# Performance work log

Hardware: AMD Instinct MI355X
Metric: run time of the kernel (lower is better)

## Reference

```python
import jax, jax.numpy as jnp
import numpy as np

B, NL2, NRC, NIN = 32768, 4, 8, 41
NCTRL = NIN + NL2 + NIN  # 86


def _blur(n):
    # tridiagonal blur: 0.8 on diag, 0.1 on the two off-diagonals (symmetric)
    return 0.8 * jnp.eye(n, dtype=jnp.float32) \
         + 0.1 * jnp.eye(n, k=1, dtype=jnp.float32) \
         + 0.1 * jnp.eye(n, k=-1, dtype=jnp.float32)


def _leaky(x):
    return jnp.where(x >= 0, x, 0.2 * x)  # LeakyReLU(0.2)


def _passgate(w, b, rc, x):
    # w: [B,out,in,rc] clamped to [-1,1]; rc: [B,rc]; x: [B,in] -> [B,out]
    w2 = jnp.einsum('boir,br->boi', jnp.clip(w, -1.0, 1.0), rc)
    return jnp.einsum('boi,bi->bo', w2, x) + b


def setup_inputs() -> dict:
    key = jax.random.key(0)
    ks = jax.random.split(key, 4)
    s_f = np.float32(np.sqrt(2.0 / (NIN * NRC)))
    s_r = np.float32(np.sqrt(2.0 / (NL2 * NRC)))
    inp = jax.random.normal(ks[0], (B, NIN), dtype=jnp.float32)
    fpg_w = jnp.clip(jax.random.normal(ks[1], (B, NL2, NIN, NRC), dtype=jnp.float32) * s_f, -1.0, 1.0)
    rpg_w = jnp.clip(jax.random.normal(ks[2], (B, NIN, NL2, NRC), dtype=jnp.float32) * s_r, -1.0, 1.0)
    fpg_b = jnp.zeros((B, NL2), dtype=jnp.float32)
    rpg_b = jnp.zeros((B, NIN), dtype=jnp.float32)
    # pgctrl: shared nn.Linear(86, 8) (default torch init ~ U(-1/sqrt(86), 1/sqrt(86)))
    bound = np.float32(1.0 / np.sqrt(NCTRL))
    kw, kb = jax.random.split(ks[3])
    pgctrl_w = jax.random.uniform(kw, (NRC, NCTRL), dtype=jnp.float32, minval=-bound, maxval=bound)
    pgctrl_b = jax.random.uniform(kb, (NRC,), dtype=jnp.float32, minval=-bound, maxval=bound)
    return {"inp": inp, "fpg_w": fpg_w, "fpg_b": fpg_b,
            "rpg_w": rpg_w, "rpg_b": rpg_b,
            "pgctrl_w": pgctrl_w, "pgctrl_b": pgctrl_b}


def reference(inp, fpg_w, fpg_b, rpg_w, rpg_b, pgctrl_w, pgctrl_b):
    rcblur = _blur(NRC)   # [8,8]
    l2blur = _blur(NL2)   # [4,4]
    # initial state buffers are zeros; note l2old/rcold are NOT updated inside
    # the outer loop (faithful to the original), only l1i carries over.
    l2old = jnp.zeros((B, NL2), dtype=inp.dtype)
    rcold = jnp.zeros((B, NRC), dtype=inp.dtype)
    l1i = jnp.zeros((B, NIN), dtype=inp.dtype)
    l2 = l2old
    rc = rcold
    for _ in range(2):
        rcin = jnp.concatenate([inp, l2old, inp - l1i], axis=1)  # [B,86]
        rc = _leaky(rcin @ pgctrl_w.T + pgctrl_b)
        rc = jnp.clip(0.4 * rc + 0.6 * rcold, -0.2, 1.0)
        for _ in range(3):
            rc = rc @ rcblur.T
        l2 = _passgate(fpg_w, fpg_b, rc, inp) * 0.1 + 0.9 * l2old
        l2 = jnp.clip(l2, -0.2, 1.0)
        for _ in range(2):
            l2 = l2 @ l2blur.T
        l1i = jnp.clip(_passgate(rpg_w, rpg_b, rc, l2), -0.2, 1.0)
    return (l1i, l2, rc)
```

## Files before the change

kernel.cpp:

```cpp
#include <hip/hip_runtime.h>

#define B_ROWS 32768
#define NIN 41
#define NL2 4
#define NRC 8

__device__ __forceinline__ float clampf(float v, float lo, float hi) {
    return fminf(fmaxf(v, lo), hi);
}

__device__ __forceinline__ float clamp1(float v) {
    return fminf(fmaxf(v, -1.f), 1.f);
}

template <int Ctrl>
__device__ __forceinline__ int dpp_add(int x) {
    return __float_as_int(
        __int_as_float(x) +
        __int_as_float(__builtin_amdgcn_update_dpp(0, x, Ctrl, 0xf, 0xf, true)));
}

__device__ __forceinline__ float wave_sum_uniform(float v) {
    int x = __float_as_int(v);
    x = dpp_add<0x111>(x);
    x = dpp_add<0x112>(x);
    x = dpp_add<0x114>(x);
    x = dpp_add<0x118>(x);
    x = dpp_add<0x142>(x);
    x = dpp_add<0x143>(x);
    return __int_as_float(__builtin_amdgcn_readlane(x, 63));
}

__global__ void __launch_bounds__(256, 4) pgnet_kernel(
    const float* __restrict__ inp,
    const float* __restrict__ fpg_w,
    const float* __restrict__ fpg_b,
    const float* __restrict__ rpg_w,
    const float* __restrict__ rpg_b,
    const float* __restrict__ pgw,
    const float* __restrict__ pgb,
    float* __restrict__ out)
{
    const int lane = threadIdx.x & 63;
    const int row  = blockIdx.x * 4 + (threadIdx.x >> 6);
    const bool act = lane < NIN;
    const int safe = act ? lane : (NIN - 1);

    const float x_raw = inp[row * NIN + safe];

    const float* fp = fpg_w + (size_t)row * 1312 + (size_t)safe * 8;
    float4 fwv[NL2][2];
    #pragma unroll
    for (int o = 0; o < NL2; ++o) {
        fwv[o][0] = *(const float4*)(fp + o * 328);
        fwv[o][1] = *(const float4*)(fp + o * 328 + 4);
    }

    const float* rp = rpg_w + (size_t)row * 1312 + (size_t)safe * 32;
    float4 rwv[8];
    #pragma unroll
    for (int j = 0; j < 8; ++j) rwv[j] = ((const float4*)rp)[j];

    float w1r[NRC], w2r[NRC];
    #pragma unroll
    for (int r = 0; r < NRC; ++r) {
        w1r[r] = pgw[r * 86 + safe];
        w2r[r] = pgw[r * 86 + 45 + safe];
    }

    const float4 fbv  = *(const float4*)(fpg_b + (size_t)row * NL2);
    const float  rb_r = rpg_b[row * NIN + safe];

    __builtin_amdgcn_sched_barrier(0);

    const float x  = act ? x_raw : 0.0f;
    const float rb = act ? rb_r  : 0.0f;

    float fw[NL2][NRC];
    #pragma unroll
    for (int o = 0; o < NL2; ++o) {
        fw[o][0] = clamp1(fwv[o][0].x); fw[o][1] = clamp1(fwv[o][0].y);
        fw[o][2] = clamp1(fwv[o][0].z); fw[o][3] = clamp1(fwv[o][0].w);
        fw[o][4] = clamp1(fwv[o][1].x); fw[o][5] = clamp1(fwv[o][1].y);
        fw[o][6] = clamp1(fwv[o][1].z); fw[o][7] = clamp1(fwv[o][1].w);
    }
    float rw[NL2][NRC];
    #pragma unroll
    for (int o = 0; o < NL2; ++o) {
        rw[o][0] = clamp1(rwv[2*o].x);   rw[o][1] = clamp1(rwv[2*o].y);
        rw[o][2] = clamp1(rwv[2*o].z);   rw[o][3] = clamp1(rwv[2*o].w);
        rw[o][4] = clamp1(rwv[2*o+1].x); rw[o][5] = clamp1(rwv[2*o+1].y);
        rw[o][6] = clamp1(rwv[2*o+1].z); rw[o][7] = clamp1(rwv[2*o+1].w);
    }

    float W2[NRC], A[NRC];
    #pragma unroll
    for (int r = 0; r < NRC; ++r) {
        W2[r] = act ? w2r[r] : 0.0f;
        A[r]  = wave_sum_uniform(x * (w1r[r] + w2r[r])) + pgb[r];
    }

    float F[NL2][NRC];
    #pragma unroll
    for (int o = 0; o < NL2; ++o)
        #pragma unroll
        for (int r = 0; r < NRC; ++r)
            F[o][r] = wave_sum_uniform(x * fw[o][r]);

    const float fb[NL2] = {fbv.x, fbv.y, fbv.z, fbv.w};

    float l1 = 0.0f;
    float rcv[NRC], l2v[NL2];

    #pragma unroll
    for (int it = 0; it < 2; ++it) {
        #pragma unroll
        for (int r = 0; r < NRC; ++r) {
            float pre = A[r];
            if (it > 0) pre -= wave_sum_uniform(l1 * W2[r]);
            float v = (pre >= 0.f) ? pre : 0.2f * pre;
            rcv[r] = clampf(0.4f * v, -0.2f, 1.0f);
        }
        #pragma unroll
        for (int t = 0; t < 3; ++t) {
            float tmp[NRC];
            #pragma unroll
            for (int r = 0; r < NRC; ++r) {
                float v = 0.8f * rcv[r];
                if (r > 0)       v += 0.1f * rcv[r - 1];
                if (r < NRC - 1) v += 0.1f * rcv[r + 1];
                tmp[r] = v;
            }
            #pragma unroll
            for (int r = 0; r < NRC; ++r) rcv[r] = tmp[r];
        }
        #pragma unroll
        for (int o = 0; o < NL2; ++o) {
            float s = fb[o];
            #pragma unroll
            for (int r = 0; r < NRC; ++r) s += F[o][r] * rcv[r];
            l2v[o] = clampf(0.1f * s, -0.2f, 1.0f);
        }
        #pragma unroll
        for (int t = 0; t < 2; ++t) {
            float tmp[NL2];
            #pragma unroll
            for (int o = 0; o < NL2; ++o) {
                float v = 0.8f * l2v[o];
                if (o > 0)       v += 0.1f * l2v[o - 1];
                if (o < NL2 - 1) v += 0.1f * l2v[o + 1];
                tmp[o] = v;
            }
            #pragma unroll
            for (int o = 0; o < NL2; ++o) l2v[o] = tmp[o];
        }
        float acc = rb;
        #pragma unroll
        for (int o = 0; o < NL2; ++o) {
            float d = 0.f;
            #pragma unroll
            for (int r = 0; r < NRC; ++r) d += rw[o][r] * rcv[r];
            acc += l2v[o] * d;
        }
        l1 = clampf(acc, -0.2f, 1.0f);
    }

    if (act) out[(size_t)row * NIN + lane] = l1;
    if (lane < NL2) {
        float v = l2v[0];
        #pragma unroll
        for (int o = 1; o < NL2; ++o) if (lane == o) v = l2v[o];
        out[(size_t)B_ROWS * NIN + (size_t)row * NL2 + lane] = v;
    }
    if (lane < NRC) {
        float v = rcv[0];
        #pragma unroll
        for (int r = 1; r < NRC; ++r) if (lane == r) v = rcv[r];
        out[(size_t)B_ROWS * (NIN + NL2) + (size_t)row * NRC + lane] = v;
    }
}

extern "C" void kernel_launch(void* const* d_in, const int* in_sizes, int n_in,
                              void* d_out, int out_size, void* d_ws, size_t ws_size,
                              hipStream_t stream) {
    const float* inp   = (const float*)d_in[0];
    const float* fpg_w = (const float*)d_in[1];
    const float* fpg_b = (const float*)d_in[2];
    const float* rpg_w = (const float*)d_in[3];
    const float* rpg_b = (const float*)d_in[4];
    const float* pgw   = (const float*)d_in[5];
    const float* pgb   = (const float*)d_in[6];
    float* out = (float*)d_out;

    dim3 grid(B_ROWS / 4);
    dim3 block(256);
    hipLaunchKernelGGL(pgnet_kernel, grid, block, 0, stream,
                       inp, fpg_w, fpg_b, rpg_w, rpg_b, pgw, pgb, out);
}
```

Measured before the change: 360.6 us.

## Defer rpg_w loads past fpg reductions, use med3 clamps, raise occupancy hint

Moves the rpg_w loads so they are issued only after the fpg_w weights have been consumed by the wave reductions. This lowers peak register pressure, and the launch bound is raised from 4 to 8 waves per SIMD. Clamps become single v_med3 instructions, and the two-iteration loop is manually unrolled into straight-line code. The risk is that the rpg_w load latency is no longer hidden behind the fpg reductions, or that the compiler spills registers under the tighter register budget.

```diff
diff --git a/kernel.cpp b/kernel.cpp
--- a/kernel.cpp
+++ b/kernel.cpp
@@ -5,12 +5,8 @@
 #define NL2 4
 #define NRC 8
 
-__device__ __forceinline__ float clampf(float v, float lo, float hi) {
-    return fminf(fmaxf(v, lo), hi);
-}
-
-__device__ __forceinline__ float clamp1(float v) {
-    return fminf(fmaxf(v, -1.f), 1.f);
+__device__ __forceinline__ float med3(float v, float lo, float hi) {
+    return __builtin_amdgcn_fmed3f(v, lo, hi);
 }
 
 template <int Ctrl>
@@ -31,7 +27,33 @@
     return __int_as_float(__builtin_amdgcn_readlane(x, 63));
 }
 
-__global__ void __launch_bounds__(256, 4) pgnet_kernel(
+__device__ __forceinline__ void blur8(float* v) {
+    float t[NRC];
+    #pragma unroll
+    for (int r = 0; r < NRC; ++r) {
+        float s = 0.8f * v[r];
+        if (r > 0)       s += 0.1f * v[r - 1];
+        if (r < NRC - 1) s += 0.1f * v[r + 1];
+        t[r] = s;
+    }
+    #pragma unroll
+    for (int r = 0; r < NRC; ++r) v[r] = t[r];
+}
+
+__device__ __forceinline__ void blur4(float* v) {
+    float t[NL2];
+    #pragma unroll
+    for (int o = 0; o < NL2; ++o) {
+        float s = 0.8f * v[o];
+        if (o > 0)       s += 0.1f * v[o - 1];
+        if (o < NL2 - 1) s += 0.1f * v[o + 1];
+        t[o] = s;
+    }
+    #pragma unroll
+    for (int o = 0; o < NL2; ++o) v[o] = t[o];
+}
+
+__global__ void __launch_bounds__(256, 8) pgnet_kernel(
     const float* __restrict__ inp,
     const float* __restrict__ fpg_w,
     const float* __restrict__ fpg_b,
@@ -48,6 +70,13 @@
 
     const float x_raw = inp[row * NIN + safe];
 
+    float w1r[NRC], w2r[NRC];
+    #pragma unroll
+    for (int r = 0; r < NRC; ++r) {
+        w1r[r] = pgw[r * 86 + safe];
+        w2r[r] = pgw[r * 86 + 45 + safe];
+    }
+
     const float* fp = fpg_w + (size_t)row * 1312 + (size_t)safe * 8;
     float4 fwv[NL2][2];
     #pragma unroll
@@ -56,104 +85,76 @@
         fwv[o][1] = *(const float4*)(fp + o * 328 + 4);
     }
 
+    const float4 fbv  = *(const float4*)(fpg_b + (size_t)row * NL2);
+    const float  rb_r = rpg_b[row * NIN + safe];
+
+    __builtin_amdgcn_sched_barrier(0);
+
+    const float x  = act ? x_raw : 0.0f;
+    const float rb = act ? rb_r  : 0.0f;
+
+    float W2[NRC], A[NRC];
+    #pragma unroll
+    for (int r = 0; r < NRC; ++r) {
+        A[r]  = wave_sum_uniform(x * (w1r[r] + w2r[r])) + pgb[r];
+        W2[r] = act ? w2r[r] : 0.0f;
+    }
+
+    float F[NL2][NRC];
+    #pragma unroll
+    for (int o = 0; o < NL2; ++o) {
+        const float f0 = x * med3(fwv[o][0].x, -1.f, 1.f);
+        const float f1 = x * med3(fwv[o][0].y, -1.f, 1.f);
+        const float f2 = x * med3(fwv[o][0].z, -1.f, 1.f);
+        const float f3 = x * med3(fwv[o][0].w, -1.f, 1.f);
+        const float f4 = x * med3(fwv[o][1].x, -1.f, 1.f);
+        const float f5 = x * med3(fwv[o][1].y, -1.f, 1.f);
+        const float f6 = x * med3(fwv[o][1].z, -1.f, 1.f);
+        const float f7 = x * med3(fwv[o][1].w, -1.f, 1.f);
+        F[o][0] = wave_sum_uniform(f0); F[o][1] = wave_sum_uniform(f1);
+        F[o][2] = wave_sum_uniform(f2); F[o][3] = wave_sum_uniform(f3);
+        F[o][4] = wave_sum_uniform(f4); F[o][5] = wave_sum_uniform(f5);
+        F[o][6] = wave_sum_uniform(f6); F[o][7] = wave_sum_uniform(f7);
+    }
+
     const float* rp = rpg_w + (size_t)row * 1312 + (size_t)safe * 32;
     float4 rwv[8];
     #pragma unroll
     for (int j = 0; j < 8; ++j) rwv[j] = ((const float4*)rp)[j];
-
-    float w1r[NRC], w2r[NRC];
-    #pragma unroll
-    for (int r = 0; r < NRC; ++r) {
-        w1r[r] = pgw[r * 86 + safe];
-        w2r[r] = pgw[r * 86 + 45 + safe];
-    }
-
-    const float4 fbv  = *(const float4*)(fpg_b + (size_t)row * NL2);
-    const float  rb_r = rpg_b[row * NIN + safe];
-
     __builtin_amdgcn_sched_barrier(0);
 
-    const float x  = act ? x_raw : 0.0f;
-    const float rb = act ? rb_r  : 0.0f;
-
-    float fw[NL2][NRC];
-    #pragma unroll
-    for (int o = 0; o < NL2; ++o) {
-        fw[o][0] = clamp1(fwv[o][0].x); fw[o][1] = clamp1(fwv[o][0].y);
-        fw[o][2] = clamp1(fwv[o][0].z); fw[o][3] = clamp1(fwv[o][0].w);
-        fw[o][4] = clamp1(fwv[o][1].x); fw[o][5] = clamp1(fwv[o][1].y);
-        fw[o][6] = clamp1(fwv[o][1].z); fw[o][7] = clamp1(fwv[o][1].w);
-    }
+    const float fb[NL2] = {fbv.x, fbv.y, fbv.z, fbv.w};
+
+    float rcv[NRC];
+    #pragma unroll
+    for (int r = 0; r < NRC; ++r) {
+        const float pre = A[r];
+        const float v = (pre >= 0.f) ? pre : 0.2f * pre;
+        rcv[r] = med3(0.4f * v, -0.2f, 1.0f);
+    }
+    blur8(rcv); blur8(rcv); blur8(rcv);
+
+    float l2v[NL2];
+    #pragma unroll
+    for (int o = 0; o < NL2; ++o) {
+        float s = fb[o];
+        #pragma unroll
+        for (int r = 0; r < NRC; ++r) s += F[o][r] * rcv[r];
+        l2v[o] = med3(0.1f * s, -0.2f, 1.0f);
+    }
+    blur4(l2v); blur4(l2v);
+
     float rw[NL2][NRC];
     #pragma unroll
     for (int o = 0; o < NL2; ++o) {
-        rw[o][0] = clamp1(rwv[2*o].x);   rw[o][1] = clamp1(rwv[2*o].y);
-        rw[o][2] = clamp1(rwv[2*o].z);   rw[o][3] = clamp1(rwv[2*o].w);
-        rw[o][4] = clamp1(rwv[2*o+1].x); rw[o][5] = clamp1(rwv[2*o+1].y);
-        rw[o][6] = clamp1(rwv[2*o+1].z); rw[o][7] = clamp1(rwv[2*o+1].w);
-    }
-
-    float W2[NRC], A[NRC];
-    #pragma unroll
-    for (int r = 0; r < NRC; ++r) {
-        W2[r] = act ? w2r[r] : 0.0f;
-        A[r]  = wave_sum_uniform(x * (w1r[r] + w2r[r])) + pgb[r];
-    }
-
-    float F[NL2][NRC];
-    #pragma unroll
-    for (int o = 0; o < NL2; ++o)
-        #pragma unroll
-        for (int r = 0; r < NRC; ++r)
-            F[o][r] = wave_sum_uniform(x * fw[o][r]);
-
-    const float fb[NL2] = {fbv.x, fbv.y, fbv.z, fbv.w};
-
-    float l1 = 0.0f;
-    float rcv[NRC], l2v[NL2];
-
-    #pragma unroll
-    for (int it = 0; it < 2; ++it) {
-        #pragma unroll
-        for (int r = 0; r < NRC; ++r) {
-            float pre = A[r];
-            if (it > 0) pre -= wave_sum_uniform(l1 * W2[r]);
-            float v = (pre >= 0.f) ? pre : 0.2f * pre;
-            rcv[r] = clampf(0.4f * v, -0.2f, 1.0f);
-        }
-        #pragma unroll
-        for (int t = 0; t < 3; ++t) {
-            float tmp[NRC];
-            #pragma unroll
-            for (int r = 0; r < NRC; ++r) {
-                float v = 0.8f * rcv[r];
-                if (r > 0)       v += 0.1f * rcv[r - 1];
-                if (r < NRC - 1) v += 0.1f * rcv[r + 1];
-                tmp[r] = v;
-            }
-            #pragma unroll
-            for (int r = 0; r < NRC; ++r) rcv[r] = tmp[r];
-        }
-        #pragma unroll
-        for (int o = 0; o < NL2; ++o) {
-            float s = fb[o];
-            #pragma unroll
-            for (int r = 0; r < NRC; ++r) s += F[o][r] * rcv[r];
-            l2v[o] = clampf(0.1f * s, -0.2f, 1.0f);
-        }
-        #pragma unroll
-        for (int t = 0; t < 2; ++t) {
-            float tmp[NL2];
-            #pragma unroll
-            for (int o = 0; o < NL2; ++o) {
-                float v = 0.8f * l2v[o];
-                if (o > 0)       v += 0.1f * l2v[o - 1];
-                if (o < NL2 - 1) v += 0.1f * l2v[o + 1];
-                tmp[o] = v;
-            }
-            #pragma unroll
-            for (int o = 0; o < NL2; ++o) l2v[o] = tmp[o];
-        }
+        rw[o][0] = med3(rwv[2*o].x, -1.f, 1.f);   rw[o][1] = med3(rwv[2*o].y, -1.f, 1.f);
+        rw[o][2] = med3(rwv[2*o].z, -1.f, 1.f);   rw[o][3] = med3(rwv[2*o].w, -1.f, 1.f);
+        rw[o][4] = med3(rwv[2*o+1].x, -1.f, 1.f); rw[o][5] = med3(rwv[2*o+1].y, -1.f, 1.f);
+        rw[o][6] = med3(rwv[2*o+1].z, -1.f, 1.f); rw[o][7] = med3(rwv[2*o+1].w, -1.f, 1.f);
+    }
+
+    float l1;
+    {
         float acc = rb;
         #pragma unroll
         for (int o = 0; o < NL2; ++o) {
@@ -162,7 +163,36 @@
             for (int r = 0; r < NRC; ++r) d += rw[o][r] * rcv[r];
             acc += l2v[o] * d;
         }
-        l1 = clampf(acc, -0.2f, 1.0f);
+        l1 = med3(acc, -0.2f, 1.0f);
+    }
+
+    #pragma unroll
+    for (int r = 0; r < NRC; ++r) {
+        const float pre = A[r] - wave_sum_uniform(l1 * W2[r]);
+        const float v = (pre >= 0.f) ? pre : 0.2f * pre;
+        rcv[r] = med3(0.4f * v, -0.2f, 1.0f);
+    }
+    blur8(rcv); blur8(rcv); blur8(rcv);
+
+    #pragma unroll
+    for (int o = 0; o < NL2; ++o) {
+        float s = fb[o];
+        #pragma unroll
+        for (int r = 0; r < NRC; ++r) s += F[o][r] * rcv[r];
+        l2v[o] = med3(0.1f * s, -0.2f, 1.0f);
+    }
+    blur4(l2v); blur4(l2v);
+
+    {
+        float acc = rb;
+        #pragma unroll
+        for (int o = 0; o < NL2; ++o) {
+            float d = 0.f;
+            #pragma unroll
+            for (int r = 0; r < NRC; ++r) d += rw[o][r] * rcv[r];
+            acc += l2v[o] * d;
+        }
+        l1 = med3(acc, -0.2f, 1.0f);
     }
 
     if (act) out[(size_t)row * NIN + lane] = l1;
```

Measured after the change: 421.8 us. 17.0% more time.
